# Kernel optimization log

Hardware: AMD Instinct MI355X
Metric: run time of the kernel (lower is better)

The kernel has to match this reference:

```python
import jax, jax.numpy as jnp
import numpy as np

SCALES = (1, 2, 4, 8, 16)
BETA = 0.25
RESI = 0.5  # Phi(embed_dim, 0.5) -> resi_ratio = 0.5


def _cubic(x):
    # PyTorch bicubic kernel, A = -0.75
    A = -0.75
    x = jnp.abs(x)
    return jnp.where(
        x <= 1.0,
        ((A + 2.0) * x - (A + 3.0)) * x * x + 1.0,
        jnp.where(x < 2.0, A * (((x - 5.0) * x + 8.0) * x - 4.0), 0.0),
    )


def _resize_axis_bicubic(x, axis, out_size):
    # Separable bicubic upsample matching F.interpolate(mode='bicubic', align_corners=False)
    in_size = x.shape[axis]
    scale = in_size / out_size
    src = (jnp.arange(out_size, dtype=jnp.float32) + 0.5) * scale - 0.5
    i0 = jnp.floor(src).astype(jnp.int32)
    frac = src - i0.astype(jnp.float32)
    offs = jnp.arange(-1, 3)
    idx = jnp.clip(i0[:, None] + offs[None, :], 0, in_size - 1)   # [out, 4]
    w = _cubic(frac[:, None] - offs[None, :].astype(jnp.float32))  # [out, 4], rows sum to 1
    g = jnp.take(x, idx, axis=axis)  # axis dim replaced by (out, 4)
    wshape = [1] * g.ndim
    wshape[axis] = out_size
    wshape[axis + 1] = 4
    return jnp.sum(g * w.reshape(wshape), axis=axis + 1)


def _bicubic(x, H, W):
    return _resize_axis_bicubic(_resize_axis_bicubic(x, 2, H), 3, W)


def _phi(x, w, b):
    # Phi: h*(1-r) + conv3x3(h)*r
    y = jax.lax.conv_general_dilated(
        x, w, (1, 1), 'SAME', dimension_numbers=('NCHW', 'OIHW', 'NCHW'))
    return x * (1.0 - RESI) + (y + b[None, :, None, None]) * RESI


def _mse(a, b):
    return jnp.mean((a - b) ** 2)


def _forward(z, emb_weight, phi_w, phi_b):
    B, C, H, W = z.shape
    K = len(SCALES)
    # PhiPartiallyShared ticks for 4 shared convs (K != 4 branch uses 1/3/K spacing)
    ticks = np.linspace(1.0 / (3.0 * 4), 1.0 - 1.0 / (3.0 * 4), 4)
    sg = jax.lax.stop_gradient
    z_d = sg(z)
    z_res = z_d
    z_hat = jnp.zeros_like(z_d)
    emb_sq = jnp.sum(emb_weight * emb_weight, axis=1)  # [n_e]
    loss = jnp.zeros((), z.dtype)
    idx_list = []
    for si, ph in enumerate(SCALES):
        if si != K - 1:
            f = H // ph  # 'area' interpolate == exact average pooling (ph divides H)
            r = z_res.reshape(B, C, ph, f, ph, f).mean(axis=(3, 5))
        else:
            r = z_res
        rf = r.transpose(0, 2, 3, 1).reshape(-1, C)  # [B*ph*ph, C]
        # argmin of cdist == argmin of ||e||^2 - 2 r.e (||r||^2 constant per row)
        d = emb_sq[None, :] - 2.0 * (rf @ emb_weight.T)  # [N, n_e]
        idx = jnp.argmin(d, axis=1)
        q = emb_weight[idx].reshape(B, ph, ph, C).transpose(0, 3, 1, 2)  # [B,C,ph,ph]
        if si != K - 1:
            q = _bicubic(q, H, W)
        pi = int(np.argmin(np.abs(ticks - si / (K - 1))))  # static Phi selection
        q = _phi(q, phi_w[pi], phi_b[pi])
        z_hat = z_hat + q
        z_res = z_res - sg(q)
        idx_list.append(idx.reshape(B, -1))
        loss = loss + BETA * _mse(sg(z_hat), z) + _mse(z_hat, z_d)
    loss = loss / K
    z_hat_st = sg(z_hat - z_d) + z  # straight-through
    return z_hat_st, loss, jnp.concatenate(idx_list, axis=1)


def setup_inputs():
    key = jax.random.key(0)
    k1, k2, k3, k4 = jax.random.split(key, 4)
    z = jax.random.normal(k1, (64, 32, 16, 16), jnp.float32)
    emb_weight = jax.random.normal(k2, (4096, 32), jnp.float32)
    phi_w = jax.random.normal(k3, (4, 32, 32, 3, 3), jnp.float32) * 0.05
    phi_b = jax.random.normal(k4, (4, 32), jnp.float32) * 0.01
    return {"z": z, "emb_weight": emb_weight, "phi_w": phi_w, "phi_b": phi_b}


def reference(z, emb_weight, phi_w, phi_b):
    return _forward(z, emb_weight, phi_w, phi_b)
```

## Files before the change

### kernel.cpp

```cpp
#include <hip/hip_runtime.h>

#define NB 64
#define NC 32
#define NH 16
#define NW 16
#define NE 4096
#define NTOT (NB*NC*NH*NW)
#define IDXW 341
#define GRID 256
#define TPB 1024

typedef float f32x2 __attribute__((ext_vector_type(2)));
typedef float f32x4 __attribute__((ext_vector_type(4)));

__device__ __forceinline__ f32x2 pkfma(f32x2 a, f32x2 b, f32x2 c) {
#if __has_builtin(__builtin_elementwise_fma)
  return __builtin_elementwise_fma(a, b, c);
#else
  return (f32x2){fmaf(a.x, b.x, c.x), fmaf(a.y, b.y, c.y)};
#endif
}

__device__ __forceinline__ double cubicw(double x) {
  const double A = -0.75;
  x = fabs(x);
  if (x <= 1.0) return ((A + 2.0) * x - (A + 3.0)) * x * x + 1.0;
  if (x < 2.0)  return A * (((x - 5.0) * x + 8.0) * x - 4.0);
  return 0.0;
}

__device__ __forceinline__ unsigned monokey(float f) {
  unsigned u = __float_as_uint(f);
  return (u & 0x80000000u) ? ~u : (u | 0x80000000u);
}

__device__ __forceinline__ unsigned aload(unsigned* p) {
  return __hip_atomic_load(p, __ATOMIC_RELAXED, __HIP_MEMORY_SCOPE_AGENT);
}

__device__ __forceinline__ void groupbar(unsigned* fl) {
  __syncthreads();
  if (threadIdx.x == 0) {
    __hip_atomic_fetch_add(fl, 1u, __ATOMIC_RELAXED, __HIP_MEMORY_SCOPE_AGENT);
    while (aload(fl) < 4u) __builtin_amdgcn_s_sleep(1);
  }
  __syncthreads();
}

__global__ __launch_bounds__(TPB)
__attribute__((amdgpu_waves_per_eu(4, 4)))
void k_fused(
    const float* __restrict__ z, const float* __restrict__ emb,
    const float* __restrict__ phi_w, const float* __restrict__ phi_b,
    double* __restrict__ rv64, double* __restrict__ emb_sq,
    double* __restrict__ loss_d, float* __restrict__ emb_ti,
    float* __restrict__ emb_sq32, int* __restrict__ win,
    unsigned* __restrict__ cnt, unsigned* __restrict__ gbar,
    unsigned* __restrict__ flags,
    float* __restrict__ out_zhat, float* __restrict__ out_loss,
    float* __restrict__ out_idx)
{
  __shared__ double lds[8192];
  char* base = (char*)lds;
  double* zres = lds;
  char* qreg   = base + 16384;
  char* ttreg  = base + 49152;

  const int tid = threadIdx.x;
  const int b = blockIdx.x & 63, jq = blockIdx.x >> 6;
  const int co0 = jq * 8;

  if (tid < 16) atomicCAS(&flags[(b << 4) + tid], 0xAAAAAAAAu, 0u);
  if (tid == 0) {
    atomicCAS((unsigned long long*)loss_d, 0xAAAAAAAAAAAAAAAAull, 0ull);
    atomicCAS(cnt, 0xAAAAAAAAu, 0u);
    atomicCAS(gbar, 0xAAAAAAAAu, 0u);
  }

  #pragma unroll
  for (int t = 0; t < 2; t++) {
    int i = t * TPB + tid;
    zres[i] = (double)z[((b * NC + co0) << 8) + i];
  }
  {
    int c0 = blockIdx.x * 16;
    if (tid < 512) {
      int cl = tid >> 5, k = tid & 31;
      emb_ti[(k >> 1) * 8192 + (c0 + cl) * 2 + (k & 1)] = emb[(c0 + cl) * NC + k];
    }
    if (tid < 16) {
      const float* er = emb + (c0 + tid) * NC;
      double s = 0.0;
      #pragma unroll
      for (int j = 0; j < 8; j++)
        s += (double)er[4*j]*er[4*j] + (double)er[4*j+1]*er[4*j+1]
           + (double)er[4*j+2]*er[4*j+2] + (double)er[4*j+3]*er[4*j+3];
      emb_sq[c0 + tid] = s;
      emb_sq32[c0 + tid] = (float)s;
    }
  }
  __syncthreads();
  if (tid == 0) {
    __threadfence();
    __hip_atomic_fetch_add(&flags[(b << 4) + 15], 1u, __ATOMIC_RELAXED,
                           __HIP_MEMORY_SCOPE_AGENT);
    if (jq == 0) {
      while (aload(&flags[(b << 4) + 15]) < 4u) __builtin_amdgcn_s_sleep(1);
      __hip_atomic_fetch_add(gbar, 1u, __ATOMIC_RELAXED,
                             __HIP_MEMORY_SCOPE_AGENT);
      while (aload(gbar) < 64u) __builtin_amdgcn_s_sleep(4);
      __hip_atomic_store(&flags[(b << 4) + 14], 1u, __ATOMIC_RELAXED,
                         __HIP_MEMORY_SCOPE_AGENT);
    } else {
      while (aload(&flags[(b << 4) + 14]) < 1u) __builtin_amdgcn_s_sleep(1);
    }
    __threadfence();
  }
  __syncthreads();

  double bloss = 0.0;
  const int pis[5]  = {0, 1, 2, 2, 3};
  const int offs[5] = {0, 1, 5, 21, 85};

  for (int si = 0; si < 5; si++) {
    const int ph = 1 << si, f = NH / ph, ph2 = ph * ph;
    const int idx_off = offs[si];

    if (si == 4) {
      #pragma unroll
      for (int t = 0; t < 2; t++) {
        int i = t * TPB + tid;
        int pix = i >> 3, cc = i & 7;
        __hip_atomic_store(&rv64[(((b << 8) + pix) << 5) + co0 + cc],
                           zres[cc * 256 + pix],
                           __ATOMIC_RELAXED, __HIP_MEMORY_SCOPE_AGENT);
      }
    } else {
      double* pp = (double*)qreg;
      double* pooled = (double*)(qreg + 8192);
      const int P = (f >= 8) ? 8 : f;
      const int lP = (f >= 8) ? 3 : ((f == 4) ? 2 : 1);
      const int items = 8 * ph2, work = items * P, dpp = f / P;
      if (tid < work) {
        int it = tid >> lP, part = tid & (P - 1);
        int cc = it >> (2 * si), rem = it & (ph2 - 1);
        int y = rem >> si, x = rem & (ph - 1);
        const double* basep = zres + cc * 256 + (y * f) * 16 + x * f;
        double s = 0.0;
        for (int dy = part * dpp; dy < part * dpp + dpp; dy++) {
          const double* rp = basep + dy * 16;
          #pragma unroll 4
          for (int dx = 0; dx < f; dx++) s += rp[dx];
        }
        pp[tid] = s;
      }
      __syncthreads();
      if (tid < items) {
        double s = 0.0;
        for (int p2 = 0; p2 < P; p2++) s += pp[(tid << lP) + p2];
        pooled[tid] = s / (double)(f * f);
      }
      __syncthreads();
      if (tid < items) {
        int rem = tid >> 3, cc = tid & 7;
        __hip_atomic_store(&rv64[(((b << 8) + rem) << 5) + co0 + cc],
                           pooled[cc * ph2 + rem],
                           __ATOMIC_RELAXED, __HIP_MEMORY_SCOPE_AGENT);
      }
    }
    groupbar(&flags[(b << 4) + si * 2]);

    {
      const int count = (ph2 > jq) ? ((ph2 - jq + 3) >> 2) : 0;
      float*  rvt32 = (float*)(base + 16384);
      double* rvt64 = (double*)(base + 24576);
      unsigned long long* wdu = (unsigned long long*)(base + 40960);
      unsigned short* cand = (unsigned short*)(base + 43008);
      for (int t = tid; t < 2048; t += TPB) {
        int m = t >> 5, k = t & 31;
        double v = __hip_atomic_load(&rv64[(((b << 8) + jq + 4 * m) << 5) + k],
                                     __ATOMIC_RELAXED, __HIP_MEMORY_SCOPE_AGENT);
        rvt64[t] = v;
        rvt32[t] = (float)v;
      }
      __syncthreads();
      if (count) {
        const int lane = tid & 63, wv_ = tid >> 6;
        for (int m0 = 0; m0 < count; m0 += 8) {
          unsigned long long p1[8], p2[8];
          #pragma unroll
          for (int j = 0; j < 8; j++) { p1[j] = ~0ull; p2[j] = ~0ull; }
          #pragma unroll
          for (int pass = 0; pass < 2; pass++) {
            const int e0 = pass * 2048 + (tid << 1);
            f32x2 acc[8];
            #pragma unroll
            for (int j = 0; j < 8; j++) acc[j] = (f32x2){0.f, 0.f};
            const f32x4* __restrict__ ebase = (const f32x4*)emb_ti + (e0 >> 1);
            #pragma unroll 4
            for (int k2 = 0; k2 < 16; k2++) {
              f32x4 E = ebase[k2 * 2048];
              #pragma unroll
              for (int j = 0; j < 8; j++) {
                f32x2 r2 = *(const f32x2*)(rvt32 + ((m0 + j) << 5) + (k2 << 1));
                acc[j] = pkfma((f32x2){r2.x, r2.x}, (f32x2){E.x, E.z}, acc[j]);
                acc[j] = pkfma((f32x2){r2.y, r2.y}, (f32x2){E.y, E.w}, acc[j]);
              }
            }
            f32x2 es = *(const f32x2*)(emb_sq32 + e0);
            #pragma unroll
            for (int j = 0; j < 8; j++) {
              float d0 = es.x - 2.f * acc[j].x;
              float d1 = es.y - 2.f * acc[j].y;
              unsigned long long k0 =
                  ((unsigned long long)monokey(d0) << 32) | (unsigned)e0;
              unsigned long long k1 =
                  ((unsigned long long)monokey(d1) << 32) | (unsigned)(e0 + 1);
              unsigned long long c1 = k0 < k1 ? k0 : k1;
              unsigned long long c2 = k0 < k1 ? k1 : k0;
              unsigned long long hi  = p1[j] < c1 ? c1 : p1[j];
              unsigned long long lo2 = p2[j] < c2 ? p2[j] : c2;
              p1[j] = p1[j] < c1 ? p1[j] : c1;
              p2[j] = hi < lo2 ? hi : lo2;
            }
          }
          #pragma unroll
          for (int j = 0; j < 8; j++) {
            unsigned long long q1v = p1[j], q2v = p2[j];
            #pragma unroll
            for (int off = 32; off >= 1; off >>= 1) {
              unsigned long long o1 = __shfl_xor(q1v, off, 64);
              unsigned long long o2 = __shfl_xor(q2v, off, 64);
              unsigned long long lo = q1v < o1 ? q1v : o1;
              unsigned long long hi = q1v < o1 ? o1 : q1v;
              unsigned long long m2 = q2v < o2 ? q2v : o2;
              q1v = lo;
              q2v = hi < m2 ? hi : m2;
            }
            if (lane == 0) {
              wdu[(wv_ << 4) + (j << 1)]     = q1v;
              wdu[(wv_ << 4) + (j << 1) + 1] = q2v;
            }
          }
          __syncthreads();
          if (tid < 8 && m0 + tid < count) {
            unsigned long long G1 = ~0ull, G2 = ~0ull;
            #pragma unroll
            for (int w = 0; w < 16; w++) {
              unsigned long long a1 = wdu[(w << 4) + (tid << 1)];
              unsigned long long a2 = wdu[(w << 4) + (tid << 1) + 1];
              if (a1 < G1) { G2 = (G1 < a2 ? G1 : a2); G1 = a1; }
              else if (a1 < G2) G2 = a1;
            }
            cand[((m0 + tid) << 1)]     = (unsigned short)(G1 & 0xFFFFu);
            cand[((m0 + tid) << 1) + 1] = (unsigned short)(G2 & 0xFFFFu);
          }
          __syncthreads();
        }
        if (tid < 2 * count) {
          int m = tid >> 1, cs = tid & 1;
          int c = cand[(m << 1) + cs];
          const float* er = emb + (c << 5);
          double dot = 0.0;
          #pragma unroll
          for (int k = 0; k < 32; k++)
            dot = fma(rvt64[(m << 5) + k], (double)er[k], dot);
          double d = emb_sq[c] - 2.0 * dot;
          double doth = __shfl_xor(d, 1, 64);
          int coth = __shfl_xor(c, 1, 64);
          if (cs == 0) {
            int wc = (doth < d || (doth == d && coth < c)) ? coth : c;
            int n = jq + (m << 2);
            __hip_atomic_store(&win[(b << 8) + n], wc,
                               __ATOMIC_RELAXED, __HIP_MEMORY_SCOPE_AGENT);
            out_idx[b * IDXW + idx_off + n] = (float)wc;
          }
        }
      }
    }
    groupbar(&flags[(b << 4) + si * 2 + 1]);

    unsigned short* fidx = (unsigned short*)(ttreg + 12800);
    if (tid < ph2)
      fidx[tid] = (unsigned short)__hip_atomic_load(&win[(b << 8) + tid],
                      __ATOMIC_RELAXED, __HIP_MEMORY_SCOPE_AGENT);
    __syncthreads();

    float* simg = (float*)qreg;
    if (si == 4) {
      for (int i = tid; i < 32 * 256; i += TPB)
        simg[i] = emb[(int)fidx[i & 255] * NC + (i >> 8)];
    } else {
      float* wtab = (float*)(ttreg + 12288);
      int* itab = (int*)(ttreg + 12544);
      double scale = (double)ph / 16.0;
      if (tid < 64) {
        int oy = tid >> 2, kk = tid & 3;
        double src = ((double)oy + 0.5) * scale - 0.5;
        double fi = floor(src);
        if (kk == 0) itab[oy] = (int)fi;
        wtab[tid] = (float)cubicw(src - fi - (double)(kk - 1));
      }
      __syncthreads();
      int CH = (si == 3) ? 16 : 32, nhalf = (si == 3) ? 2 : 1;
      float* qs = (float*)(ttreg + 8192);
      float* tt = (float*)ttreg;
      for (int half = 0; half < nhalf; half++) {
        int c0 = half * CH;
        for (int i = tid; i < CH * ph2; i += TPB) {
          int cc = i >> (2 * si), rem = i & (ph2 - 1);
          qs[i] = emb[(int)fidx[rem] * NC + c0 + cc];
        }
        __syncthreads();
        for (int i = tid; i < CH * 16 * ph; i += TPB) {
          int x = i & (ph - 1), oy = (i >> si) & 15, cc = i >> (4 + si);
          int i0 = itab[oy];
          float s = 0.f;
          #pragma unroll
          for (int k = 0; k < 4; k++) {
            int iy = min(max(i0 + k - 1, 0), ph - 1);
            s = fmaf(wtab[oy * 4 + k], qs[(cc * ph + iy) * ph + x], s);
          }
          tt[i] = s;
        }
        __syncthreads();
        for (int i = tid; i < CH * 256; i += TPB) {
          int ox = i & 15, oy = (i >> 4) & 15, cc = i >> 8;
          int i0 = itab[ox];
          float s = 0.f;
          #pragma unroll
          for (int k = 0; k < 4; k++) {
            int ix = min(max(i0 + k - 1, 0), ph - 1);
            s = fmaf(wtab[ox * 4 + k], tt[(cc * 16 + oy) * ph + ix], s);
          }
          simg[(c0 + cc) * 256 + oy * 16 + ox] = s;
        }
        __syncthreads();
      }
    }
    __syncthreads();

    {
      float* lw2 = (float*)ttreg;
      const float* wsrc = phi_w + (pis[si] * NC + co0) * NC * 9;
      for (int i = tid; i < 2304; i += TPB) {
        int co = i / 288, rem = i - co * 288;
        lw2[(((co >> 1) * 288 + rem) << 1) + (co & 1)] = wsrc[i];
      }
      __syncthreads();
      int pix = tid & 255, sub = tid >> 8;
      int x = pix & 15, y = pix >> 4;
      f32x2 a = {0.f, 0.f};
      const f32x2* wp = (const f32x2*)lw2 + sub * 288;
      for (int ci = 0; ci < NC; ci++) {
        float wv[9];
        #pragma unroll
        for (int ky = 0; ky < 3; ky++) {
          int yy = y + ky - 1;
          #pragma unroll
          for (int kx = 0; kx < 3; kx++) {
            int xx = x + kx - 1;
            wv[ky * 3 + kx] = (yy >= 0 && yy < NH && xx >= 0 && xx < NW)
                              ? simg[(ci << 8) + yy * 16 + xx] : 0.f;
          }
        }
        #pragma unroll
        for (int k = 0; k < 9; k++)
          a = pkfma((f32x2){wv[k], wv[k]}, wp[ci * 9 + k], a);
      }
      double lsum = 0.0;
      #pragma unroll
      for (int jj = 0; jj < 2; jj++) {
        int col = (sub << 1) + jj;
        float aj = jj ? a.y : a.x;
        float val = simg[((co0 + col) << 8) + pix] * 0.5f
                  + (aj + phi_b[pis[si] * NC + co0 + col]) * 0.5f;
        int li = (col << 8) + pix;
        double zr = zres[li] - (double)val;
        zres[li] = zr;
        if (si == 4) {
          int gi = ((b * NC + co0 + col) << 8) + pix;
          out_zhat[gi] = (float)((double)z[gi] - zr);
        }
        lsum += zr * zr;
      }
      __syncthreads();
      #pragma unroll
      for (int off = 32; off >= 1; off >>= 1)
        lsum += __shfl_xor(lsum, off, 64);
      double* red = (double*)qreg;
      if ((tid & 63) == 0) red[tid >> 6] = lsum;
      __syncthreads();
      if (tid < 16) {
        double v = red[tid];
        #pragma unroll
        for (int off = 8; off >= 1; off >>= 1) v += __shfl_xor(v, off, 16);
        if (tid == 0) bloss += v;
      }
      __syncthreads();
    }
  }

  if (tid == 0) {
    double old = unsafeAtomicAdd(loss_d, bloss); (void)old;
    asm volatile("s_waitcnt vmcnt(0)" ::: "memory");
    unsigned n = __hip_atomic_fetch_add(cnt, 1u, __ATOMIC_RELAXED,
                                        __HIP_MEMORY_SCOPE_AGENT);
    if (n == GRID - 1u) {
      double tot = __hip_atomic_load(loss_d, __ATOMIC_RELAXED,
                                     __HIP_MEMORY_SCOPE_AGENT);
      *out_loss = (float)(tot * (1.25 / (5.0 * (double)NTOT)));
    }
  }
}

extern "C" void kernel_launch(void* const* d_in, const int* in_sizes, int n_in,
                              void* d_out, int out_size, void* d_ws, size_t ws_size,
                              hipStream_t stream) {
  const float* z     = (const float*)d_in[0];
  const float* emb   = (const float*)d_in[1];
  const float* phi_w = (const float*)d_in[2];
  const float* phi_b = (const float*)d_in[3];

  float* out      = (float*)d_out;
  float* out_zhat = out;
  float* out_loss = out + NTOT;
  float* out_idx  = out + NTOT + 1;

  double* ws       = (double*)d_ws;
  double* rv64     = ws;
  double* emb_sq   = rv64 + 64 * 256 * NC;
  double* loss_d   = emb_sq + NE;
  float*  emb_ti   = (float*)(loss_d + 2);
  float*  emb_sq32 = emb_ti + NE * NC;
  int*    win      = (int*)(emb_sq32 + NE);
  unsigned* cnt    = (unsigned*)(win + NB * 256);
  unsigned* gbar   = cnt + 1;
  unsigned* flags  = gbar + 1;

  k_fused<<<GRID, TPB, 0, stream>>>(z, emb, phi_w, phi_b,
                                    rv64, emb_sq, loss_d, emb_ti, emb_sq32,
                                    win, cnt, gbar, flags,
                                    out_zhat, out_loss, out_idx);
}
```

Before: 499.8 us.

## Split nearest-code search across codebook halves and row halves per batch group

Changes how the four blocks of each batch divide the argmin search. Previously each block handled an interleaved quarter of rows and scanned the whole codebook in two passes. Now each block takes one codebook half and one row half, and writes top-2 candidates to global workspace. After an extra group barrier, every block redundantly refines four candidates per row in fp64 reading rv64 from global memory. This balances work better at small scales and halves per-block codebook streaming, at the cost of one more group barrier per scale and more global atomic traffic.

```diff
diff --git a/kernel.cpp b/kernel.cpp
--- a/kernel.cpp
+++ b/kernel.cpp
@@ -37,6 +37,9 @@
 __device__ __forceinline__ unsigned aload(unsigned* p) {
   return __hip_atomic_load(p, __ATOMIC_RELAXED, __HIP_MEMORY_SCOPE_AGENT);
 }
+__device__ __forceinline__ double aloadd(double* p) {
+  return __hip_atomic_load(p, __ATOMIC_RELAXED, __HIP_MEMORY_SCOPE_AGENT);
+}
 
 __device__ __forceinline__ void groupbar(unsigned* fl) {
   __syncthreads();
@@ -54,7 +57,7 @@
     const float* __restrict__ phi_w, const float* __restrict__ phi_b,
     double* __restrict__ rv64, double* __restrict__ emb_sq,
     double* __restrict__ loss_d, float* __restrict__ emb_ti,
-    float* __restrict__ emb_sq32, int* __restrict__ win,
+    float* __restrict__ emb_sq32, unsigned* __restrict__ cand_ws,
     unsigned* __restrict__ cnt, unsigned* __restrict__ gbar,
     unsigned* __restrict__ flags,
     float* __restrict__ out_zhat, float* __restrict__ out_loss,
@@ -69,8 +72,9 @@
   const int tid = threadIdx.x;
   const int b = blockIdx.x & 63, jq = blockIdx.x >> 6;
   const int co0 = jq * 8;
-
-  if (tid < 16) atomicCAS(&flags[(b << 4) + tid], 0xAAAAAAAAu, 0u);
+  const int ch = jq & 1, rh = jq >> 1;
+
+  if (tid < 32) atomicCAS(&flags[(b << 5) + tid], 0xAAAAAAAAu, 0u);
   if (tid == 0) {
     atomicCAS((unsigned long long*)loss_d, 0xAAAAAAAAAAAAAAAAull, 0ull);
     atomicCAS(cnt, 0xAAAAAAAAu, 0u);
@@ -102,17 +106,17 @@
   __syncthreads();
   if (tid == 0) {
     __threadfence();
-    __hip_atomic_fetch_add(&flags[(b << 4) + 15], 1u, __ATOMIC_RELAXED,
+    __hip_atomic_fetch_add(&flags[(b << 5) + 31], 1u, __ATOMIC_RELAXED,
                            __HIP_MEMORY_SCOPE_AGENT);
     if (jq == 0) {
-      while (aload(&flags[(b << 4) + 15]) < 4u) __builtin_amdgcn_s_sleep(1);
+      while (aload(&flags[(b << 5) + 31]) < 4u) __builtin_amdgcn_s_sleep(1);
       __hip_atomic_fetch_add(gbar, 1u, __ATOMIC_RELAXED,
                              __HIP_MEMORY_SCOPE_AGENT);
       while (aload(gbar) < 64u) __builtin_amdgcn_s_sleep(4);
-      __hip_atomic_store(&flags[(b << 4) + 14], 1u, __ATOMIC_RELAXED,
+      __hip_atomic_store(&flags[(b << 5) + 30], 1u, __ATOMIC_RELAXED,
                          __HIP_MEMORY_SCOPE_AGENT);
     } else {
-      while (aload(&flags[(b << 4) + 14]) < 1u) __builtin_amdgcn_s_sleep(1);
+      while (aload(&flags[(b << 5) + 30]) < 1u) __builtin_amdgcn_s_sleep(1);
     }
     __threadfence();
   }
@@ -168,82 +172,69 @@
                            __ATOMIC_RELAXED, __HIP_MEMORY_SCOPE_AGENT);
       }
     }
-    groupbar(&flags[(b << 4) + si * 2]);
+    groupbar(&flags[(b << 5) + si * 3]);
 
     {
-      const int count = (ph2 > jq) ? ((ph2 - jq + 3) >> 2) : 0;
-      float*  rvt32 = (float*)(base + 16384);
-      double* rvt64 = (double*)(base + 24576);
-      unsigned long long* wdu = (unsigned long long*)(base + 40960);
-      unsigned short* cand = (unsigned short*)(base + 43008);
-      for (int t = tid; t < 2048; t += TPB) {
+      const int half = (ph2 + 1) >> 1;
+      int rows_start = rh * half; if (rows_start > ph2) rows_start = ph2;
+      int rows_end = rows_start + half; if (rows_end > ph2) rows_end = ph2;
+      const int nrows = rows_end - rows_start;
+      float* rvt32 = (float*)(base + 16384);
+      unsigned long long* wdu = (unsigned long long*)(base + 32768);
+      const int nstage = (nrows + 7) & ~7;
+      for (int t = tid; t < nstage * 32; t += TPB) {
         int m = t >> 5, k = t & 31;
-        double v = __hip_atomic_load(&rv64[(((b << 8) + jq + 4 * m) << 5) + k],
-                                     __ATOMIC_RELAXED, __HIP_MEMORY_SCOPE_AGENT);
-        rvt64[t] = v;
-        rvt32[t] = (float)v;
-      }
-      __syncthreads();
-      if (count) {
+        int n = rows_start + m; if (n > ph2 - 1) n = ph2 - 1;
+        rvt32[t] = (float)aloadd(&rv64[(((b << 8) + n) << 5) + k]);
+      }
+      __syncthreads();
+      if (nrows) {
+        const int e0 = ch * 2048 + (tid << 1);
+        const f32x2 es = *(const f32x2*)(emb_sq32 + e0);
         const int lane = tid & 63, wv_ = tid >> 6;
-        for (int m0 = 0; m0 < count; m0 += 8) {
-          unsigned long long p1[8], p2[8];
+        const f32x4* __restrict__ ebase =
+            (const f32x4*)emb_ti + (ch ? 1024 : 0) + tid;
+        for (int m0 = 0; m0 < nrows; m0 += 8) {
+          f32x2 acc[8];
           #pragma unroll
-          for (int j = 0; j < 8; j++) { p1[j] = ~0ull; p2[j] = ~0ull; }
-          #pragma unroll
-          for (int pass = 0; pass < 2; pass++) {
-            const int e0 = pass * 2048 + (tid << 1);
-            f32x2 acc[8];
-            #pragma unroll
-            for (int j = 0; j < 8; j++) acc[j] = (f32x2){0.f, 0.f};
-            const f32x4* __restrict__ ebase = (const f32x4*)emb_ti + (e0 >> 1);
-            #pragma unroll 4
-            for (int k2 = 0; k2 < 16; k2++) {
-              f32x4 E = ebase[k2 * 2048];
-              #pragma unroll
-              for (int j = 0; j < 8; j++) {
-                f32x2 r2 = *(const f32x2*)(rvt32 + ((m0 + j) << 5) + (k2 << 1));
-                acc[j] = pkfma((f32x2){r2.x, r2.x}, (f32x2){E.x, E.z}, acc[j]);
-                acc[j] = pkfma((f32x2){r2.y, r2.y}, (f32x2){E.y, E.w}, acc[j]);
-              }
-            }
-            f32x2 es = *(const f32x2*)(emb_sq32 + e0);
+          for (int j = 0; j < 8; j++) acc[j] = (f32x2){0.f, 0.f};
+          #pragma unroll 4
+          for (int k2 = 0; k2 < 16; k2++) {
+            f32x4 E = ebase[k2 * 2048];
             #pragma unroll
             for (int j = 0; j < 8; j++) {
-              float d0 = es.x - 2.f * acc[j].x;
-              float d1 = es.y - 2.f * acc[j].y;
-              unsigned long long k0 =
-                  ((unsigned long long)monokey(d0) << 32) | (unsigned)e0;
-              unsigned long long k1 =
-                  ((unsigned long long)monokey(d1) << 32) | (unsigned)(e0 + 1);
-              unsigned long long c1 = k0 < k1 ? k0 : k1;
-              unsigned long long c2 = k0 < k1 ? k1 : k0;
-              unsigned long long hi  = p1[j] < c1 ? c1 : p1[j];
-              unsigned long long lo2 = p2[j] < c2 ? p2[j] : c2;
-              p1[j] = p1[j] < c1 ? p1[j] : c1;
-              p2[j] = hi < lo2 ? hi : lo2;
+              f32x2 r2 = *(const f32x2*)(rvt32 + ((m0 + j) << 5) + (k2 << 1));
+              acc[j] = pkfma((f32x2){r2.x, r2.x}, (f32x2){E.x, E.z}, acc[j]);
+              acc[j] = pkfma((f32x2){r2.y, r2.y}, (f32x2){E.y, E.w}, acc[j]);
             }
           }
           #pragma unroll
           for (int j = 0; j < 8; j++) {
-            unsigned long long q1v = p1[j], q2v = p2[j];
+            float d0 = es.x - 2.f * acc[j].x;
+            float d1 = es.y - 2.f * acc[j].y;
+            unsigned long long k0 =
+                ((unsigned long long)monokey(d0) << 32) | (unsigned)e0;
+            unsigned long long k1 =
+                ((unsigned long long)monokey(d1) << 32) | (unsigned)(e0 + 1);
+            unsigned long long p1 = k0 < k1 ? k0 : k1;
+            unsigned long long p2 = k0 < k1 ? k1 : k0;
             #pragma unroll
             for (int off = 32; off >= 1; off >>= 1) {
-              unsigned long long o1 = __shfl_xor(q1v, off, 64);
-              unsigned long long o2 = __shfl_xor(q2v, off, 64);
-              unsigned long long lo = q1v < o1 ? q1v : o1;
-              unsigned long long hi = q1v < o1 ? o1 : q1v;
-              unsigned long long m2 = q2v < o2 ? q2v : o2;
-              q1v = lo;
-              q2v = hi < m2 ? hi : m2;
+              unsigned long long q1 = __shfl_xor(p1, off, 64);
+              unsigned long long q2 = __shfl_xor(p2, off, 64);
+              unsigned long long lo = p1 < q1 ? p1 : q1;
+              unsigned long long hi = p1 < q1 ? q1 : p1;
+              unsigned long long m2 = p2 < q2 ? p2 : q2;
+              p1 = lo;
+              p2 = hi < m2 ? hi : m2;
             }
             if (lane == 0) {
-              wdu[(wv_ << 4) + (j << 1)]     = q1v;
-              wdu[(wv_ << 4) + (j << 1) + 1] = q2v;
+              wdu[(wv_ << 4) + (j << 1)]     = p1;
+              wdu[(wv_ << 4) + (j << 1) + 1] = p2;
             }
           }
           __syncthreads();
-          if (tid < 8 && m0 + tid < count) {
+          if (tid < 8 && m0 + tid < nrows) {
             unsigned long long G1 = ~0ull, G2 = ~0ull;
             #pragma unroll
             for (int w = 0; w < 16; w++) {
@@ -252,39 +243,46 @@
               if (a1 < G1) { G2 = (G1 < a2 ? G1 : a2); G1 = a1; }
               else if (a1 < G2) G2 = a1;
             }
-            cand[((m0 + tid) << 1)]     = (unsigned short)(G1 & 0xFFFFu);
-            cand[((m0 + tid) << 1) + 1] = (unsigned short)(G2 & 0xFFFFu);
+            int n = rows_start + m0 + tid;
+            unsigned* cw = cand_ws + (((((b << 1) + ch) << 8) + n) << 1);
+            __hip_atomic_store(&cw[0], (unsigned)(G1 & 0xFFFFu),
+                               __ATOMIC_RELAXED, __HIP_MEMORY_SCOPE_AGENT);
+            __hip_atomic_store(&cw[1], (unsigned)(G2 & 0xFFFFu),
+                               __ATOMIC_RELAXED, __HIP_MEMORY_SCOPE_AGENT);
           }
           __syncthreads();
         }
-        if (tid < 2 * count) {
-          int m = tid >> 1, cs = tid & 1;
-          int c = cand[(m << 1) + cs];
-          const float* er = emb + (c << 5);
-          double dot = 0.0;
-          #pragma unroll
-          for (int k = 0; k < 32; k++)
-            dot = fma(rvt64[(m << 5) + k], (double)er[k], dot);
-          double d = emb_sq[c] - 2.0 * dot;
-          double doth = __shfl_xor(d, 1, 64);
-          int coth = __shfl_xor(c, 1, 64);
-          if (cs == 0) {
-            int wc = (doth < d || (doth == d && coth < c)) ? coth : c;
-            int n = jq + (m << 2);
-            __hip_atomic_store(&win[(b << 8) + n], wc,
-                               __ATOMIC_RELAXED, __HIP_MEMORY_SCOPE_AGENT);
-            out_idx[b * IDXW + idx_off + n] = (float)wc;
-          }
-        }
-      }
-    }
-    groupbar(&flags[(b << 4) + si * 2 + 1]);
-
+      }
+    }
+    groupbar(&flags[(b << 5) + si * 3 + 1]);
+
+    {
+      unsigned short* fidx = (unsigned short*)(ttreg + 12800);
+      if (tid < 4 * ph2) {
+        int n = tid >> 2, cs = tid & 3;
+        int c = (int)aload(&cand_ws[(((((b << 1) + (cs >> 1)) << 8) + n) << 1)
+                                    + (cs & 1)]);
+        const float* er = emb + (c << 5);
+        double* rrow = rv64 + (((b << 8) + n) << 5);
+        double dot = 0.0;
+        #pragma unroll
+        for (int k = 0; k < 32; k++)
+          dot = fma(aloadd(&rrow[k]), (double)er[k], dot);
+        double d = emb_sq[c] - 2.0 * dot;
+        #pragma unroll
+        for (int off = 1; off <= 2; off <<= 1) {
+          double od = __shfl_xor(d, off, 64);
+          int oc = __shfl_xor(c, off, 64);
+          if (od < d || (od == d && oc < c)) { d = od; c = oc; }
+        }
+        if (cs == 0) {
+          fidx[n] = (unsigned short)c;
+          if (jq == 0) out_idx[b * IDXW + idx_off + n] = (float)c;
+        }
+      }
+    }
+    groupbar(&flags[(b << 5) + si * 3 + 2]);
     unsigned short* fidx = (unsigned short*)(ttreg + 12800);
-    if (tid < ph2)
-      fidx[tid] = (unsigned short)__hip_atomic_load(&win[(b << 8) + tid],
-                      __ATOMIC_RELAXED, __HIP_MEMORY_SCOPE_AGENT);
-    __syncthreads();
 
     float* simg = (float*)qreg;
     if (si == 4) {
@@ -305,8 +303,8 @@
       int CH = (si == 3) ? 16 : 32, nhalf = (si == 3) ? 2 : 1;
       float* qs = (float*)(ttreg + 8192);
       float* tt = (float*)ttreg;
-      for (int half = 0; half < nhalf; half++) {
-        int c0 = half * CH;
+      for (int hlf = 0; hlf < nhalf; hlf++) {
+        int c0 = hlf * CH;
         for (int i = tid; i < CH * ph2; i += TPB) {
           int cc = i >> (2 * si), rem = i & (ph2 - 1);
           qs[i] = emb[(int)fidx[rem] * NC + c0 + cc];
@@ -427,19 +425,19 @@
   float* out_loss = out + NTOT;
   float* out_idx  = out + NTOT + 1;
 
-  double* ws       = (double*)d_ws;
-  double* rv64     = ws;
-  double* emb_sq   = rv64 + 64 * 256 * NC;
-  double* loss_d   = emb_sq + NE;
-  float*  emb_ti   = (float*)(loss_d + 2);
-  float*  emb_sq32 = emb_ti + NE * NC;
-  int*    win      = (int*)(emb_sq32 + NE);
-  unsigned* cnt    = (unsigned*)(win + NB * 256);
-  unsigned* gbar   = cnt + 1;
-  unsigned* flags  = gbar + 1;
+  double* ws        = (double*)d_ws;
+  double* rv64      = ws;
+  double* emb_sq    = rv64 + 64 * 256 * NC;
+  double* loss_d    = emb_sq + NE;
+  float*  emb_ti    = (float*)(loss_d + 2);
+  float*  emb_sq32  = emb_ti + NE * NC;
+  unsigned* cand_ws = (unsigned*)(emb_sq32 + NE);
+  unsigned* cnt     = cand_ws + 64 * 2 * 256 * 2;
+  unsigned* gbar    = cnt + 1;
+  unsigned* flags   = gbar + 1;
 
   k_fused<<<GRID, TPB, 0, stream>>>(z, emb, phi_w, phi_b,
                                     rv64, emb_sq, loss_d, emb_ti, emb_sq32,
-                                    win, cnt, gbar, flags,
+                                    cand_ws, cnt, gbar, flags,
                                     out_zhat, out_loss, out_idx);
 }
```

New measurement: 697.1 us. 1.39x slower.
